# Kernel tuning notes

Hardware: AMD Instinct MI355X
Metric: run time of the kernel (lower is better)

Reference implementation:

```python
import jax, jax.numpy as jnp
import numpy as np

BIG = 1e10  # sentinel depth for empty pixels


def setup_inputs() -> dict:
    key = jax.random.key(0)
    k1, k2, k3, k4, k5 = jax.random.split(key, 5)
    N, C = 200000, 64
    B, H, W = 4, 376, 1241
    features = jax.random.normal(k1, (N, C), dtype=jnp.float32)
    # coordinates: [batch_id, z, y, x]; grid is ~67 bins per axis given
    # voxel_size=0.75 and pcd_range [0,-25,-25,50,25,25]
    b = jax.random.randint(k2, (N, 1), 0, B, dtype=jnp.int32)
    z = jax.random.randint(k3, (N, 1), 0, 67, dtype=jnp.int32)
    y = jax.random.randint(k4, (N, 1), 0, 67, dtype=jnp.int32)
    x = jax.random.randint(k5, (N, 1), 0, 67, dtype=jnp.int32)
    coordinates = jnp.concatenate([b, z, y, x], axis=1)
    # KITTI-like pinhole intrinsics
    K = jnp.array([[721.5377, 0.0, 609.5593],
                   [0.0, 721.5377, 172.854],
                   [0.0, 0.0, 1.0]], dtype=jnp.float32)
    return {"features": features, "coordinates": coordinates, "K": K,
            "batch_size": B, "h": H, "w": W}


def _projection_matrix(K):
    # module-constant R and V2P (from __init__ defaults)
    R = jnp.array([[0., -1., 0.], [0., 0., -1.], [1., 0., 0.]], dtype=jnp.float32)
    vx = vy = vz = 0.75
    x_off = vx / 2 + 0.0
    y_off = vy / 2 + (-25.0)
    z_off = vz / 2 + (-25.0)
    V2P = jnp.array([[vx, 0., 0., x_off],
                     [0., vy, 0., y_off],
                     [0., 0., vz, z_off]], dtype=jnp.float32)
    return K @ R @ V2P  # [3,4]


def reference(features, coordinates, K, batch_size, h, w):
    N, C = features.shape
    P = _projection_matrix(K)  # [3,4]
    b = coordinates[:, 0]
    # coordinates order is [batch_id, z, y, x]; homogeneous point is [x,y,z,1]
    xyz1 = jnp.stack([coordinates[:, 3], coordinates[:, 2], coordinates[:, 1],
                      jnp.ones_like(coordinates[:, 0])], axis=1).astype(jnp.float32)
    p = xyz1 @ P.T  # [N,3]
    depth = p[:, 2]
    safe_d = jnp.where(depth > 1e-6, depth, 1.0)
    u = jnp.floor(p[:, 0] / safe_d).astype(jnp.int32)
    v = jnp.floor(p[:, 1] / safe_d).astype(jnp.int32)
    valid = (depth > 1e-6) & (u >= 0) & (u < w) & (v >= 0) & (v < h)
    num_pix = batch_size * h * w
    pix = jnp.where(valid, b * (h * w) + v * w + u, 0)
    d = jnp.where(valid, depth, BIG)
    # z-buffer: min depth per pixel, then winning voxel index (tie -> smallest idx)
    min_depth = jnp.full((num_pix,), BIG, dtype=jnp.float32).at[pix].min(d)
    is_win = valid & (d <= min_depth[pix])
    cand = jnp.where(is_win, jnp.arange(N, dtype=jnp.int32), N)
    win_idx = jnp.full((num_pix,), N, dtype=jnp.int32).at[pix].min(cand)
    feats_pad = jnp.concatenate([features, jnp.zeros((1, C), features.dtype)], axis=0)
    out = feats_pad[win_idx].reshape(batch_size, h, w, C).transpose(0, 3, 1, 2)  # [B,C,H,W]
    inv_depth = jnp.where(min_depth < BIG, 1.0 / min_depth, 0.0).reshape(batch_size, h, w)
    return out, inv_depth
```

## Files before the change

### kernel.cpp

```cpp
#include <hip/hip_runtime.h>
#include <cstdint>
#include <cstddef>

constexpr int Bc = 4;
constexpr int Hc = 376;
constexpr int Wc = 1241;
constexpr int Cc = 64;
constexpr int HW = Hc * Wc;
constexpr int NUM_PIX = Bc * HW;
constexpr int TILE = 64;
constexpr int PAD = 65;
constexpr int NTILES = (NUM_PIX + TILE - 1) / TILE;


__global__ void init_entries(uint4* __restrict__ p, int n16) {
    int t = blockIdx.x * blockDim.x + threadIdx.x;
    if (t < n16) p[t] = make_uint4(0xFFFFFFFFu, 0xFFFFFFFFu, 0xFFFFFFFFu, 0xFFFFFFFFu);
}

__global__ void scatter_points(const int* __restrict__ coords,
                               const float* __restrict__ Km,
                               unsigned long long* __restrict__ entries,
                               int N) {
    int n = blockIdx.x * blockDim.x + threadIdx.x;
    if (n >= N) return;

    const int4 co = *(const int4*)(coords + 4 * (size_t)n);
    const int   bi = co.x;
    const float zf = (float)co.y;
    const float yf = (float)co.z;
    const float xf = (float)co.w;

    float P0[4], P1[4], P2[4];
    {
        const float xo = 0.375f, yo = -24.625f, zo = -24.625f;
        float KR0, KR1, KR2;
        KR0 = Km[2]; KR1 = -Km[0]; KR2 = -Km[1];
        P0[0] = __fmaf_rn(KR0, 0.75f, 0.0f);
        P0[1] = __fmaf_rn(KR1, 0.75f, 0.0f);
        P0[2] = __fmaf_rn(KR2, 0.75f, 0.0f);
        P0[3] = __fmaf_rn(KR2, zo, __fmaf_rn(KR1, yo, __fmaf_rn(KR0, xo, 0.0f)));
        KR0 = Km[5]; KR1 = -Km[3]; KR2 = -Km[4];
        P1[0] = __fmaf_rn(KR0, 0.75f, 0.0f);
        P1[1] = __fmaf_rn(KR1, 0.75f, 0.0f);
        P1[2] = __fmaf_rn(KR2, 0.75f, 0.0f);
        P1[3] = __fmaf_rn(KR2, zo, __fmaf_rn(KR1, yo, __fmaf_rn(KR0, xo, 0.0f)));
        KR0 = Km[8]; KR1 = -Km[6]; KR2 = -Km[7];
        P2[0] = __fmaf_rn(KR0, 0.75f, 0.0f);
        P2[1] = __fmaf_rn(KR1, 0.75f, 0.0f);
        P2[2] = __fmaf_rn(KR2, 0.75f, 0.0f);
        P2[3] = __fmaf_rn(KR2, zo, __fmaf_rn(KR1, yo, __fmaf_rn(KR0, xo, 0.0f)));
    }

    float p0 = __fmaf_rn(1.0f, P0[3], __fmaf_rn(zf, P0[2], __fmaf_rn(yf, P0[1], __fmaf_rn(xf, P0[0], 0.0f))));
    float p1 = __fmaf_rn(1.0f, P1[3], __fmaf_rn(zf, P1[2], __fmaf_rn(yf, P1[1], __fmaf_rn(xf, P1[0], 0.0f))));
    float depth = __fmaf_rn(1.0f, P2[3], __fmaf_rn(zf, P2[2], __fmaf_rn(yf, P2[1], __fmaf_rn(xf, P2[0], 0.0f))));

    const bool dok = depth > 1e-6f;
    const float safe_d = dok ? depth : 1.0f;
    const int u = (int)floorf(__fdiv_rn(p0, safe_d));
    const int v = (int)floorf(__fdiv_rn(p1, safe_d));

    if (dok && u >= 0 && u < Wc && v >= 0 && v < Hc && bi >= 0 && bi < Bc) {
        const int pix = bi * HW + v * Wc + u;
        const unsigned long long key =
            ((unsigned long long)__float_as_uint(depth) << 32) | (unsigned int)n;
        atomicMin(&entries[pix], key);
    }
}

__global__ __launch_bounds__(256, 2)
void gather_tile(const unsigned long long* __restrict__ entries,
                 const float* __restrict__ feat,
                 float* __restrict__ out_feat,
                 float* __restrict__ out_inv) {
    __shared__ float smem[TILE * PAD];
    __shared__ int   s_idx[TILE];

    const int tid  = threadIdx.x;
    const int wave = tid >> 6;
    const int lane = tid & 63;
    const int g0   = blockIdx.x * TILE;

    if (tid < TILE) {
        int idx = -1;
        if (g0 + tid < NUM_PIX) {
            const unsigned long long e = entries[g0 + tid];
            float inv = 0.0f;
            if (e != ~0ULL) {
                idx = (int)(unsigned int)(e & 0xFFFFFFFFu);
                inv = __fdiv_rn(1.0f, __uint_as_float((unsigned int)(e >> 32)));
            }
            out_inv[g0 + tid] = inv;
        }
        s_idx[tid] = idx;
    }
    __syncthreads();

    const float4* feat4 = (const float4*)feat;
    const int j = lane & 15;
    for (int it = 0; it < 4; ++it) {
        const int p = (wave * 4 + it) * 4 + (lane >> 4);
        const int idx = s_idx[p];
        float4 v = make_float4(0.f, 0.f, 0.f, 0.f);
        if (idx >= 0) v = feat4[(size_t)idx * 16 + j];
        float* row = smem + p * PAD + 4 * j;
        row[0] = v.x; row[1] = v.y; row[2] = v.z; row[3] = v.w;
    }
    __syncthreads();

    const int g = g0 + lane;
    if (g < NUM_PIX) {
        const int b = g / HW;
        const int local = g - b * HW;
        float* outBase = out_feat + (size_t)b * Cc * HW + local;
        for (int i = 0; i < 16; ++i) {
            const int c = wave * 16 + i;
            outBase[(size_t)c * HW] = smem[lane * PAD + c];
        }
    }
}

extern "C" void kernel_launch(void* const* d_in, const int* in_sizes, int n_in,
                              void* d_out, int out_size, void* d_ws, size_t ws_size,
                              hipStream_t stream) {
    const float* features = (const float*)d_in[0];
    const int*   coords   = (const int*)d_in[1];
    const float* Km       = (const float*)d_in[2];
    const int N = in_sizes[1] / 4;

    unsigned long long* entries = (unsigned long long*)d_ws;

    float* out_feat = (float*)d_out;
    float* out_inv  = (float*)d_out + (size_t)Bc * Cc * HW;

    const int n16 = NUM_PIX / 2;
    init_entries<<<(n16 + 255) / 256, 256, 0, stream>>>((uint4*)entries, n16);

    scatter_points<<<(N + 255) / 256, 256, 0, stream>>>(coords, Km, entries, N);

    gather_tile<<<NTILES, 256, 0, stream>>>(entries, features, out_feat, out_inv);
}
```

Before: 586.7 us.

## Vectorize feature-map stores with float4 and widen the gather tile to 128 pixels

The gather kernel now handles 128 pixels per block. Each thread writes four consecutive pixels of one channel as a single float4, so the dominant output write to the planar [B,C,H,W] tensor uses wider stores. Feature rows are now loaded by two threads per pixel with unrolled float4 reads, which makes the read side less coalesced across a wavefront. The custom init kernel is replaced by hipMemsetAsync. The occupancy hint in the launch bounds is dropped.

```diff
diff --git a/kernel.cpp b/kernel.cpp
--- a/kernel.cpp
+++ b/kernel.cpp
@@ -8,15 +8,11 @@
 constexpr int Cc = 64;
 constexpr int HW = Hc * Wc;
 constexpr int NUM_PIX = Bc * HW;
-constexpr int TILE = 64;
-constexpr int PAD = 65;
+
+constexpr int TILE = 128;
+constexpr int PADS = 65;
 constexpr int NTILES = (NUM_PIX + TILE - 1) / TILE;
 
-
-__global__ void init_entries(uint4* __restrict__ p, int n16) {
-    int t = blockIdx.x * blockDim.x + threadIdx.x;
-    if (t < n16) p[t] = make_uint4(0xFFFFFFFFu, 0xFFFFFFFFu, 0xFFFFFFFFu, 0xFFFFFFFFu);
-}
 
 __global__ void scatter_points(const int* __restrict__ coords,
                                const float* __restrict__ Km,
@@ -69,54 +65,71 @@
     }
 }
 
-__global__ __launch_bounds__(256, 2)
+__global__ __launch_bounds__(256)
 void gather_tile(const unsigned long long* __restrict__ entries,
                  const float* __restrict__ feat,
                  float* __restrict__ out_feat,
                  float* __restrict__ out_inv) {
-    __shared__ float smem[TILE * PAD];
+    __shared__ float smem[TILE * PADS];
     __shared__ int   s_idx[TILE];
 
-    const int tid  = threadIdx.x;
-    const int wave = tid >> 6;
-    const int lane = tid & 63;
-    const int g0   = blockIdx.x * TILE;
+    const int tid = threadIdx.x;
+    const int g0  = blockIdx.x * TILE;
 
     if (tid < TILE) {
         int idx = -1;
-        if (g0 + tid < NUM_PIX) {
-            const unsigned long long e = entries[g0 + tid];
+        const int g = g0 + tid;
+        if (g < NUM_PIX) {
+            const unsigned long long e = entries[g];
             float inv = 0.0f;
             if (e != ~0ULL) {
                 idx = (int)(unsigned int)(e & 0xFFFFFFFFu);
                 inv = __fdiv_rn(1.0f, __uint_as_float((unsigned int)(e >> 32)));
             }
-            out_inv[g0 + tid] = inv;
+            out_inv[g] = inv;
         }
         s_idx[tid] = idx;
     }
     __syncthreads();
 
-    const float4* feat4 = (const float4*)feat;
-    const int j = lane & 15;
-    for (int it = 0; it < 4; ++it) {
-        const int p = (wave * 4 + it) * 4 + (lane >> 4);
-        const int idx = s_idx[p];
-        float4 v = make_float4(0.f, 0.f, 0.f, 0.f);
-        if (idx >= 0) v = feat4[(size_t)idx * 16 + j];
-        float* row = smem + p * PAD + 4 * j;
-        row[0] = v.x; row[1] = v.y; row[2] = v.z; row[3] = v.w;
+    {
+        const int p    = tid >> 1;
+        const int half = tid & 1;
+        const int idx  = s_idx[p];
+        const float4* fr = (const float4*)(feat + (size_t)(idx < 0 ? 0 : idx) * Cc);
+        float* row = smem + p * PADS;
+        #pragma unroll
+        for (int it = 0; it < 8; ++it) {
+            const int j = half * 8 + it;
+            float4 v = make_float4(0.f, 0.f, 0.f, 0.f);
+            if (idx >= 0) v = fr[j];
+            row[4 * j + 0] = v.x;
+            row[4 * j + 1] = v.y;
+            row[4 * j + 2] = v.z;
+            row[4 * j + 3] = v.w;
+        }
     }
     __syncthreads();
 
-    const int g = g0 + lane;
-    if (g < NUM_PIX) {
-        const int b = g / HW;
-        const int local = g - b * HW;
-        float* outBase = out_feat + (size_t)b * Cc * HW + local;
-        for (int i = 0; i < 16; ++i) {
-            const int c = wave * 16 + i;
-            outBase[(size_t)c * HW] = smem[lane * PAD + c];
+    {
+        const int slot  = tid & 31;
+        const int cbase = (tid >> 5) * 8;
+        const int gq    = g0 + 4 * slot;
+        if (gq < NUM_PIX) {
+            const int b     = gq / HW;
+            const int local = gq - b * HW;
+            float* o0 = out_feat + (size_t)b * Cc * HW + local;
+            const float* s0 = smem + 4 * slot * PADS;
+            #pragma unroll
+            for (int i = 0; i < 8; ++i) {
+                const int c = cbase + i;
+                float4 v;
+                v.x = s0[0 * PADS + c];
+                v.y = s0[1 * PADS + c];
+                v.z = s0[2 * PADS + c];
+                v.w = s0[3 * PADS + c];
+                *(float4*)(o0 + (size_t)c * HW) = v;
+            }
         }
     }
 }
@@ -134,8 +147,7 @@
     float* out_feat = (float*)d_out;
     float* out_inv  = (float*)d_out + (size_t)Bc * Cc * HW;
 
-    const int n16 = NUM_PIX / 2;
-    init_entries<<<(n16 + 255) / 256, 256, 0, stream>>>((uint4*)entries, n16);
+    hipMemsetAsync(entries, 0xFF, (size_t)NUM_PIX * 8, stream);
 
     scatter_points<<<(N + 255) / 256, 256, 0, stream>>>(coords, Km, entries, N);
 
```

After: 584.2 us. About the same (-0.4%).
